# Optimization experiments

Hardware: AMD Instinct MI355X
Metric: run time of the kernel (lower is better)

The kernel has to match this reference:

```python
import jax, jax.numpy as jnp
import numpy as np

# Master-Slave MoE: dense shared 'master' expert Mlp applied to every token,
# plus num_experts 'slave' Mlp experts combined via top-k softmax gating,
# output = master(x) + sum_k gate_k * expert_k(x). Each Mlp: fc2(gelu(fc1(x))).

DIM = 512
HID = 4 * DIM
NUM_EXPERTS = 8
TOP_K = 2


def mlp(x, w1, b1, w2, b2):
    h = jax.nn.gelu(jnp.einsum('bnd,dh->bnh', x, w1) + b1)
    return jnp.einsum('bnh,hd->bnd', h, w2) + b2


def setup_inputs() -> dict:
    key = jax.random.key(0)
    ks = jax.random.split(key, 10)
    B, N = 4, 4096
    s1 = 1.0 / np.sqrt(DIM)
    s2 = 1.0 / np.sqrt(HID)
    return {
        'x': jax.random.normal(ks[0], (B, N, DIM), jnp.float32),
        'gate_w': jax.random.normal(ks[1], (DIM, NUM_EXPERTS), jnp.float32) * s1,
        'master_w1': jax.random.normal(ks[2], (DIM, HID), jnp.float32) * s1,
        'master_b1': jnp.zeros((HID,), jnp.float32),
        'master_w2': jax.random.normal(ks[3], (HID, DIM), jnp.float32) * s2,
        'master_b2': jnp.zeros((DIM,), jnp.float32),
        'expert_w1': jax.random.normal(ks[4], (NUM_EXPERTS, DIM, HID), jnp.float32) * s1,
        'expert_b1': jnp.zeros((NUM_EXPERTS, HID), jnp.float32),
        'expert_w2': jax.random.normal(ks[5], (NUM_EXPERTS, HID, DIM), jnp.float32) * s2,
        'expert_b2': jnp.zeros((NUM_EXPERTS, DIM), jnp.float32),
    }


def reference(x, gate_w, master_w1, master_b1, master_w2, master_b2,
              expert_w1, expert_b1, expert_w2, expert_b2):
    B, N, D = x.shape
    # Router: top-k softmax gating over experts
    logits = jnp.einsum('bnd,de->bne', x, gate_w)  # [B,N,E]
    topv, topi = jax.lax.top_k(logits, TOP_K)       # [B,N,K]
    gates_k = jax.nn.softmax(topv, axis=-1)         # [B,N,K]
    # dense gate matrix [B,N,E] (zeros for non-selected experts)
    gates = jnp.zeros_like(logits)
    gates = jnp.take_along_axis(gates, topi, axis=-1)  # noop to keep shape clarity
    gates = jnp.zeros_like(logits).at[
        jnp.arange(B)[:, None, None],
        jnp.arange(N)[None, :, None],
        topi].set(gates_k)

    # Master (shared) expert applied to all tokens
    master_out = mlp(x, master_w1, master_b1, master_w2, master_b2)

    # Slave experts: compute per-expert Mlp (vectorized over experts),
    # combine with gate weights. Gate is sparse (only top-k nonzero),
    # mathematically equal to token routing.
    h = jax.nn.gelu(jnp.einsum('bnd,edh->ebnh', x, expert_w1)
                    + expert_b1[:, None, None, :])          # [E,B,N,H]
    eo = jnp.einsum('ebnh,ehd->ebnd', h, expert_w2) \
         + expert_b2[:, None, None, :]                       # [E,B,N,D]
    slave_out = jnp.einsum('bne,ebnd->bnd', gates, eo)

    return master_out + slave_out
```

## Files before the change

### kernel.cpp

```cpp
#include <hip/hip_runtime.h>

#define DIM 512
#define HID 2048
#define NE 8

typedef _Float16 half8v __attribute__((ext_vector_type(8)));
typedef _Float16 half4v __attribute__((ext_vector_type(4)));
typedef float f32x4 __attribute__((ext_vector_type(4)));

__device__ __forceinline__ void gload16(const void* g, void* l) {
  __builtin_amdgcn_global_load_lds(
      (const __attribute__((address_space(1))) void*)g,
      (__attribute__((address_space(3))) void*)l, 16, 0, 0);
}

__global__ void k_cast_fp16(const float* __restrict__ src, _Float16* __restrict__ dst, int n4) {
  int i = blockIdx.x * blockDim.x + threadIdx.x;
  int stride = gridDim.x * blockDim.x;
  for (; i < n4; i += stride) {
    float4 v = ((const float4*)src)[i];
    half4v h = { (_Float16)v.x, (_Float16)v.y, (_Float16)v.z, (_Float16)v.w };
    ((half4v*)dst)[i] = h;
  }
}

__global__ void k_transpose_cast(const float* __restrict__ src, _Float16* __restrict__ dst,
                                 int R, int C) {
  __shared__ _Float16 ts[64][66];
  int z = blockIdx.z;
  src += (size_t)z * R * C;
  dst += (size_t)z * R * C;
  int c0 = blockIdx.x * 64, r0 = blockIdx.y * 64;
  int t = threadIdx.x;
  int rr = t >> 4, cc = (t & 15) * 4;
  #pragma unroll
  for (int i = 0; i < 4; i++) {
    int row = rr + i * 16;
    float4 v = *(const float4*)&src[(size_t)(r0 + row) * C + c0 + cc];
    ts[row][cc + 0] = (_Float16)v.x; ts[row][cc + 1] = (_Float16)v.y;
    ts[row][cc + 2] = (_Float16)v.z; ts[row][cc + 3] = (_Float16)v.w;
  }
  __syncthreads();
  int cr = t >> 4, rb = (t & 15) * 4;
  #pragma unroll
  for (int i = 0; i < 4; i++) {
    int c = cr + i * 16;
    half4v o = { ts[rb + 0][c], ts[rb + 1][c], ts[rb + 2][c], ts[rb + 3][c] };
    *(half4v*)&dst[(size_t)(c0 + c) * R + r0 + rb] = o;
  }
}

#define RT_TOK 16
__global__ void k_router(const float* __restrict__ x, const float* __restrict__ gw,
                         int* __restrict__ counts, int* __restrict__ perm,
                         float* __restrict__ pgate, int T) {
  __shared__ float xs[RT_TOK][520];
  __shared__ float gwt[8][520];
  __shared__ float lg[RT_TOK][8];
  int t = threadIdx.x;
  int tk0 = blockIdx.x * RT_TOK;
  for (int i = t; i < DIM * NE; i += 128) {
    int k = i >> 3, e = i & 7;
    gwt[e][k] = gw[i];
  }
  for (int i = t; i < RT_TOK * (DIM / 4); i += 128) {
    int row = i / (DIM / 4); int c4 = i % (DIM / 4);
    float4 v = *(const float4*)&x[(size_t)(tk0 + row) * DIM + c4 * 4];
    xs[row][c4 * 4 + 0] = v.x; xs[row][c4 * 4 + 1] = v.y;
    xs[row][c4 * 4 + 2] = v.z; xs[row][c4 * 4 + 3] = v.w;
  }
  __syncthreads();
  int tok = t >> 3, e = t & 7;
  float acc = 0.f;
  for (int k = 0; k < DIM; k += 4) {
    float4 xv = *(const float4*)&xs[tok][k];
    float4 wv = *(const float4*)&gwt[e][k];
    acc += xv.x * wv.x + xv.y * wv.y + xv.z * wv.z + xv.w * wv.w;
  }
  lg[tok][e] = acc;
  __syncthreads();
  if (t < RT_TOK) {
    float v0 = -1e30f, v1 = -1e30f; int i0 = 0, i1 = 0;
    #pragma unroll
    for (int j = 0; j < 8; j++) { float v = lg[t][j]; if (v > v0) { v0 = v; i0 = j; } }
    #pragma unroll
    for (int j = 0; j < 8; j++) { if (j == i0) continue; float v = lg[t][j]; if (v > v1) { v1 = v; i1 = j; } }
    float g0 = 1.f / (1.f + __expf(v1 - v0));
    float g1 = 1.f - g0;
    int token = tk0 + t;
    int p0 = atomicAdd(&counts[i0], 1);
    perm[i0 * T + p0] = token; pgate[i0 * T + p0] = g0;
    int p1 = atomicAdd(&counts[i1], 1);
    perm[i1 * T + p1] = token; pgate[i1 * T + p1] = g1;
  }
}

__global__ void k_offsets(const int* __restrict__ counts, int* __restrict__ offsets) {
  if (threadIdx.x == 0) {
    int s = 0;
    for (int e = 0; e < 8; e++) { offsets[e] = s; s += counts[e]; }
  }
}


__device__ __forceinline__ void compute_tile(const _Float16* Asb, const _Float16* Bsb,
                                             int wm, int wn, int lane, int rb,
                                             f32x4 acc[4][4]) {
  const char* ab = (const char*)Asb;
  const char* bb = (const char*)Bsb;
  half8v af[4], bf[4];
  #pragma unroll
  for (int mi = 0; mi < 4; mi++)
    af[mi] = *(const half8v*)(ab + ((wm + mi * 16) << 6) + rb);
  #pragma unroll
  for (int ni = 0; ni < 4; ni++)
    bf[ni] = *(const half8v*)(bb + ((wn + ni * 16) << 6) + rb);
  #pragma unroll
  for (int mi = 0; mi < 4; mi++)
    #pragma unroll
    for (int ni = 0; ni < 4; ni++)
      acc[mi][ni] = __builtin_amdgcn_mfma_f32_16x16x32_f16(af[mi], bf[ni], acc[mi][ni], 0, 0, 0);
}

template<int K, int MODE>
__global__ __launch_bounds__(256) void k_gemm(
    const _Float16* __restrict__ A,
    const _Float16* __restrict__ Bt,
    const float* __restrict__ bias,
    int bias_stride,
    const int* __restrict__ counts,
    int count_fixed,
    const int* __restrict__ offsets,
    const int* __restrict__ perm,
    const float* __restrict__ pgate,
    _Float16* __restrict__ hout,
    float* __restrict__ out,
    int T) {
  constexpr int N = (MODE == 0) ? HID : DIM;
  constexpr int KT = K / 32;
  int e = blockIdx.z;
  int count = counts ? counts[e] : count_fixed;
  int m0 = blockIdx.x * 128;
  if (m0 >= count) return;
  int n0 = blockIdx.y * 128;
  int hbase = offsets ? offsets[e] : 0;
  const _Float16* Be = Bt + (size_t)e * N * K;
  const float* be = bias + (size_t)e * bias_stride;

  __shared__ _Float16 As[2][128 * 32];
  __shared__ _Float16 Bs[2][128 * 32];

  int t = threadIdx.x;
  int lane = t & 63;
  int wid = t >> 6;
  int wm = (wid & 1) * 64, wn = (wid >> 1) * 64;

  const char* aSrc0; const char* aSrc1; const char* bSrc0; const char* bSrc1;
  {
    int s0 = t,        r0a = s0 >> 2, cg0 = (s0 & 3) ^ ((r0a + (r0a >> 2)) & 3);
    int s1 = t + 256,  r1a = s1 >> 2, cg1 = (s1 & 3) ^ ((r1a + (r1a >> 2)) & 3);
    int pos0 = m0 + r0a; int pr0 = pos0 < count ? pos0 : count - 1;
    int pos1 = m0 + r1a; int pr1 = pos1 < count ? pos1 : count - 1;
    int arow0, arow1;
    if (MODE == 0) { arow0 = perm ? perm[e * T + pr0] : pr0; arow1 = perm ? perm[e * T + pr1] : pr1; }
    else           { arow0 = hbase + pr0; arow1 = hbase + pr1; }
    aSrc0 = (const char*)(A + (size_t)arow0 * K) + cg0 * 16;
    aSrc1 = (const char*)(A + (size_t)arow1 * K) + cg1 * 16;
    bSrc0 = (const char*)(Be + (size_t)(n0 + r0a) * K) + cg0 * 16;
    bSrc1 = (const char*)(Be + (size_t)(n0 + r1a) * K) + cg1 * 16;
  }

  int cR = (lane >> 4) ^ (((lane & 3) + ((lane >> 2) & 3)) & 3);
  int rb = ((lane & 15) << 6) + (cR << 4);

  f32x4 acc[4][4] = {};

#define STAGE(buf, off) do { \
    gload16(aSrc0 + (off), (char*)As[buf] + t * 16); \
    gload16(aSrc1 + (off), (char*)As[buf] + t * 16 + 4096); \
    gload16(bSrc0 + (off), (char*)Bs[buf] + t * 16); \
    gload16(bSrc1 + (off), (char*)Bs[buf] + t * 16 + 4096); \
  } while (0)

  STAGE(0, 0);
  for (int kt = 0; kt < KT; kt += 2) {
    STAGE(1, (kt + 1) * 64);
    asm volatile("s_waitcnt vmcnt(4)" ::: "memory");
    __builtin_amdgcn_s_barrier();
    __builtin_amdgcn_sched_barrier(0);
    compute_tile(As[0], Bs[0], wm, wn, lane, rb, acc);
    __builtin_amdgcn_sched_barrier(0);
    __builtin_amdgcn_s_barrier();
    if (kt + 2 < KT) {
      STAGE(0, (kt + 2) * 64);
      asm volatile("s_waitcnt vmcnt(4)" ::: "memory");
    } else {
      asm volatile("s_waitcnt vmcnt(0)" ::: "memory");
    }
    __builtin_amdgcn_s_barrier();
    __builtin_amdgcn_sched_barrier(0);
    compute_tile(As[1], Bs[1], wm, wn, lane, rb, acc);
    __builtin_amdgcn_sched_barrier(0);
    __builtin_amdgcn_s_barrier();
  }
#undef STAGE

  int cl = lane & 15, rh = (lane >> 4) * 4;
  float bv[4];
  #pragma unroll
  for (int ni = 0; ni < 4; ni++) bv[ni] = be[n0 + wn + ni * 16 + cl];
  #pragma unroll
  for (int mi = 0; mi < 4; mi++) {
    #pragma unroll
    for (int r = 0; r < 4; r++) {
      int pos = m0 + wm + mi * 16 + rh + r;
      if (pos >= count) continue;
      int orow; float g = 1.f;
      if (MODE == 0) orow = hbase + pos;
      else {
        orow = perm ? perm[e * T + pos] : pos;
        if (MODE == 2) g = pgate[e * T + pos];
      }
      #pragma unroll
      for (int ni = 0; ni < 4; ni++) {
        float v = acc[mi][ni][r] + bv[ni];
        int col = n0 + wn + ni * 16 + cl;
        if (MODE == 0) {
          float ge = v / (1.f + __expf(-1.5957691216057308f * (v + 0.044715f * v * v * v)));
          hout[(size_t)orow * HID + col] = (_Float16)ge;
        } else if (MODE == 1) {
          out[(size_t)orow * DIM + col] = v;
        } else {
          unsafeAtomicAdd(&out[(size_t)orow * DIM + col], g * v);
        }
      }
    }
  }
}

extern "C" void kernel_launch(void* const* d_in, const int* in_sizes, int n_in,
                              void* d_out, int out_size, void* d_ws, size_t ws_size,
                              hipStream_t stream) {
  const float* x         = (const float*)d_in[0];
  const float* gate_w    = (const float*)d_in[1];
  const float* master_w1 = (const float*)d_in[2];
  const float* master_b1 = (const float*)d_in[3];
  const float* master_w2 = (const float*)d_in[4];
  const float* master_b2 = (const float*)d_in[5];
  const float* expert_w1 = (const float*)d_in[6];
  const float* expert_b1 = (const float*)d_in[7];
  const float* expert_w2 = (const float*)d_in[8];
  const float* expert_b2 = (const float*)d_in[9];
  float* out = (float*)d_out;
  int T = in_sizes[0] / DIM;

  char* p = (char*)d_ws;
  _Float16* xb   = (_Float16*)p; p += (size_t)T * DIM * 2;
  _Float16* wb1t = (_Float16*)p; p += (size_t)9 * HID * DIM * 2;
  _Float16* wb2t = (_Float16*)p; p += (size_t)9 * DIM * HID * 2;
  int*   counts  = (int*)p;      p += 256;
  int*   offsets = (int*)p;      p += 256;
  int*   perm    = (int*)p;      p += (size_t)8 * T * 4;
  float* pgate   = (float*)p;    p += (size_t)8 * T * 4;
  _Float16* hbuf = (_Float16*)p; p += (size_t)2 * T * HID * 2;

  hipMemsetAsync(counts, 0, 64, stream);

  k_cast_fp16<<<1024, 256, 0, stream>>>(x, xb, T * DIM / 4);

  k_transpose_cast<<<dim3(HID / 64, DIM / 64, 8), 256, 0, stream>>>(expert_w1, wb1t, DIM, HID);
  k_transpose_cast<<<dim3(HID / 64, DIM / 64, 1), 256, 0, stream>>>(master_w1, wb1t + (size_t)8 * HID * DIM, DIM, HID);
  k_transpose_cast<<<dim3(DIM / 64, HID / 64, 8), 256, 0, stream>>>(expert_w2, wb2t, HID, DIM);
  k_transpose_cast<<<dim3(DIM / 64, HID / 64, 1), 256, 0, stream>>>(master_w2, wb2t + (size_t)8 * DIM * HID, HID, DIM);

  k_router<<<T / RT_TOK, 128, 0, stream>>>(x, gate_w, counts, perm, pgate, T);
  k_offsets<<<1, 64, 0, stream>>>(counts, offsets);

  k_gemm<DIM, 0><<<dim3(T / 128, HID / 128, 1), 256, 0, stream>>>(
      xb, wb1t + (size_t)8 * HID * DIM, master_b1, 0, nullptr, T, nullptr, nullptr, nullptr,
      hbuf, nullptr, T);
  k_gemm<HID, 1><<<dim3(T / 128, DIM / 128, 1), 256, 0, stream>>>(
      hbuf, wb2t + (size_t)8 * DIM * HID, master_b2, 0, nullptr, T, nullptr, nullptr, nullptr,
      nullptr, out, T);

  k_gemm<DIM, 0><<<dim3(T / 128, HID / 128, 8), 256, 0, stream>>>(
      xb, wb1t, expert_b1, HID, counts, 0, offsets, perm, nullptr,
      hbuf, nullptr, T);
  k_gemm<HID, 2><<<dim3(T / 128, DIM / 128, 8), 256, 0, stream>>>(
      hbuf, wb2t, expert_b2, DIM, counts, 0, offsets, perm, pgate,
      nullptr, out, T);
}
```

Baseline: 603.4 us.

## Merge master and expert GEMMs into single 9-group launches and restructure pipeline

Treats the master MLP as a ninth expert group so that fc1 and fc2 each run as one grouped launch instead of two. The master's hidden activations go into an enlarged hidden buffer at offset 2T, the output is zeroed with a memset, and all fc2 results are accumulated atomically. The K-loop is also reworked: each tile's compute is issued right after the next stage's loads, with a full vmcnt(0) wait before every barrier. The aim is to cut launch overhead and tail effects and to fill the machine better. The cost is an extra memset, atomics for the master output, and a different load/compute overlap pattern.

```diff
diff --git a/kernel.cpp b/kernel.cpp
--- a/kernel.cpp
+++ b/kernel.cpp
@@ -95,16 +95,18 @@
   }
 }
 
-__global__ void k_offsets(const int* __restrict__ counts, int* __restrict__ offsets) {
+__global__ void k_offsets(int* __restrict__ counts, int* __restrict__ offsets, int T) {
   if (threadIdx.x == 0) {
     int s = 0;
     for (int e = 0; e < 8; e++) { offsets[e] = s; s += counts[e]; }
+    counts[8] = T;
+    offsets[8] = 2 * T;
   }
 }
 
 
 __device__ __forceinline__ void compute_tile(const _Float16* Asb, const _Float16* Bsb,
-                                             int wm, int wn, int lane, int rb,
+                                             int wm, int wn, int rb,
                                              f32x4 acc[4][4]) {
   const char* ab = (const char*)Asb;
   const char* bb = (const char*)Bsb;
@@ -126,10 +128,9 @@
 __global__ __launch_bounds__(256) void k_gemm(
     const _Float16* __restrict__ A,
     const _Float16* __restrict__ Bt,
-    const float* __restrict__ bias,
-    int bias_stride,
+    const float* __restrict__ ebias,
+    const float* __restrict__ mbias,
     const int* __restrict__ counts,
-    int count_fixed,
     const int* __restrict__ offsets,
     const int* __restrict__ perm,
     const float* __restrict__ pgate,
@@ -139,13 +140,14 @@
   constexpr int N = (MODE == 0) ? HID : DIM;
   constexpr int KT = K / 32;
   int e = blockIdx.z;
-  int count = counts ? counts[e] : count_fixed;
+  bool isM = (e == NE);
+  int count = counts[e];
   int m0 = blockIdx.x * 128;
   if (m0 >= count) return;
   int n0 = blockIdx.y * 128;
-  int hbase = offsets ? offsets[e] : 0;
+  int hbase = offsets[e];
   const _Float16* Be = Bt + (size_t)e * N * K;
-  const float* be = bias + (size_t)e * bias_stride;
+  const float* be = isM ? mbias : ebias + (size_t)e * N;
 
   __shared__ _Float16 As[2][128 * 32];
   __shared__ _Float16 Bs[2][128 * 32];
@@ -162,8 +164,12 @@
     int pos0 = m0 + r0a; int pr0 = pos0 < count ? pos0 : count - 1;
     int pos1 = m0 + r1a; int pr1 = pos1 < count ? pos1 : count - 1;
     int arow0, arow1;
-    if (MODE == 0) { arow0 = perm ? perm[e * T + pr0] : pr0; arow1 = perm ? perm[e * T + pr1] : pr1; }
-    else           { arow0 = hbase + pr0; arow1 = hbase + pr1; }
+    if (MODE == 0) {
+      arow0 = isM ? pr0 : perm[e * T + pr0];
+      arow1 = isM ? pr1 : perm[e * T + pr1];
+    } else {
+      arow0 = hbase + pr0; arow1 = hbase + pr1;
+    }
     aSrc0 = (const char*)(A + (size_t)arow0 * K) + cg0 * 16;
     aSrc1 = (const char*)(A + (size_t)arow1 * K) + cg1 * 16;
     bSrc0 = (const char*)(Be + (size_t)(n0 + r0a) * K) + cg0 * 16;
@@ -183,25 +189,22 @@
   } while (0)
 
   STAGE(0, 0);
+  asm volatile("s_waitcnt vmcnt(0)" ::: "memory");
+  __builtin_amdgcn_s_barrier();
+
   for (int kt = 0; kt < KT; kt += 2) {
-    STAGE(1, (kt + 1) * 64);
-    asm volatile("s_waitcnt vmcnt(4)" ::: "memory");
+    if (kt + 1 < KT) STAGE(1, (kt + 1) * 64);
+    compute_tile(As[0], Bs[0], wm, wn, rb, acc);
+    __builtin_amdgcn_sched_barrier(0);
+    asm volatile("s_waitcnt vmcnt(0)" ::: "memory");
     __builtin_amdgcn_s_barrier();
-    __builtin_amdgcn_sched_barrier(0);
-    compute_tile(As[0], Bs[0], wm, wn, lane, rb, acc);
-    __builtin_amdgcn_sched_barrier(0);
-    __builtin_amdgcn_s_barrier();
-    if (kt + 2 < KT) {
-      STAGE(0, (kt + 2) * 64);
-      asm volatile("s_waitcnt vmcnt(4)" ::: "memory");
-    } else {
+    if (kt + 2 < KT) STAGE(0, (kt + 2) * 64);
+    if (kt + 1 < KT) {
+      compute_tile(As[1], Bs[1], wm, wn, rb, acc);
+      __builtin_amdgcn_sched_barrier(0);
       asm volatile("s_waitcnt vmcnt(0)" ::: "memory");
+      __builtin_amdgcn_s_barrier();
     }
-    __builtin_amdgcn_s_barrier();
-    __builtin_amdgcn_sched_barrier(0);
-    compute_tile(As[1], Bs[1], wm, wn, lane, rb, acc);
-    __builtin_amdgcn_sched_barrier(0);
-    __builtin_amdgcn_s_barrier();
   }
 #undef STAGE
 
@@ -218,8 +221,8 @@
       int orow; float g = 1.f;
       if (MODE == 0) orow = hbase + pos;
       else {
-        orow = perm ? perm[e * T + pos] : pos;
-        if (MODE == 2) g = pgate[e * T + pos];
+        orow = isM ? pos : perm[e * T + pos];
+        if (!isM) g = pgate[e * T + pos];
       }
       #pragma unroll
       for (int ni = 0; ni < 4; ni++) {
@@ -228,8 +231,6 @@
         if (MODE == 0) {
           float ge = v / (1.f + __expf(-1.5957691216057308f * (v + 0.044715f * v * v * v)));
           hout[(size_t)orow * HID + col] = (_Float16)ge;
-        } else if (MODE == 1) {
-          out[(size_t)orow * DIM + col] = v;
         } else {
           unsafeAtomicAdd(&out[(size_t)orow * DIM + col], g * v);
         }
@@ -262,9 +263,10 @@
   int*   offsets = (int*)p;      p += 256;
   int*   perm    = (int*)p;      p += (size_t)8 * T * 4;
   float* pgate   = (float*)p;    p += (size_t)8 * T * 4;
-  _Float16* hbuf = (_Float16*)p; p += (size_t)2 * T * HID * 2;
+  _Float16* hbuf = (_Float16*)p; p += (size_t)3 * T * HID * 2;
 
   hipMemsetAsync(counts, 0, 64, stream);
+  hipMemsetAsync(out, 0, (size_t)T * DIM * 4, stream);
 
   k_cast_fp16<<<1024, 256, 0, stream>>>(x, xb, T * DIM / 4);
 
@@ -274,19 +276,12 @@
   k_transpose_cast<<<dim3(DIM / 64, HID / 64, 1), 256, 0, stream>>>(master_w2, wb2t + (size_t)8 * DIM * HID, HID, DIM);
 
   k_router<<<T / RT_TOK, 128, 0, stream>>>(x, gate_w, counts, perm, pgate, T);
-  k_offsets<<<1, 64, 0, stream>>>(counts, offsets);
-
-  k_gemm<DIM, 0><<<dim3(T / 128, HID / 128, 1), 256, 0, stream>>>(
-      xb, wb1t + (size_t)8 * HID * DIM, master_b1, 0, nullptr, T, nullptr, nullptr, nullptr,
+  k_offsets<<<1, 64, 0, stream>>>(counts, offsets, T);
+
+  k_gemm<DIM, 0><<<dim3(T / 128, HID / 128, 9), 256, 0, stream>>>(
+      xb, wb1t, expert_b1, master_b1, counts, offsets, perm, nullptr,
       hbuf, nullptr, T);
-  k_gemm<HID, 1><<<dim3(T / 128, DIM / 128, 1), 256, 0, stream>>>(
-      hbuf, wb2t + (size_t)8 * DIM * HID, master_b2, 0, nullptr, T, nullptr, nullptr, nullptr,
+  k_gemm<HID, 2><<<dim3(T / 128, DIM / 128, 9), 256, 0, stream>>>(
+      hbuf, wb2t, expert_b2, master_b2, counts, offsets, perm, pgate,
       nullptr, out, T);
-
-  k_gemm<DIM, 0><<<dim3(T / 128, HID / 128, 8), 256, 0, stream>>>(
-      xb, wb1t, expert_b1, HID, counts, 0, offsets, perm, nullptr,
-      hbuf, nullptr, T);
-  k_gemm<HID, 2><<<dim3(T / 128, DIM / 128, 8), 256, 0, stream>>>(
-      hbuf, wb2t, expert_b2, DIM, counts, 0, offsets, perm, pgate,
-      nullptr, out, T);
-}
+}
```

Result: slower. 767.2 us (+27.1%).
